# Optimization experiments

Measured on AMD Instinct MI355X. Metric: run time of the kernel, lower is better.

The kernel has to match this reference:

```python
import jax, jax.numpy as jnp
import numpy as np

EPS = 1e-5
HIDDEN = 32

def layer_norm(x, gamma, beta):
    mu = jnp.mean(x, axis=-1, keepdims=True)
    var = jnp.mean(jnp.square(x - mu), axis=-1, keepdims=True)
    return (x - mu) * jax.lax.rsqrt(var + EPS) * gamma + beta

def setup_inputs() -> dict:
    key = jax.random.key(0)
    ks = jax.random.split(key, 5)
    dim, hidden, out_dim = 256, HIDDEN, 128
    B, L = 1, 384
    x = jax.random.normal(ks[0], (B, L, dim), dtype=jnp.float32)
    gamma = jnp.ones((dim,), dtype=jnp.float32)
    beta = jnp.zeros((dim,), dtype=jnp.float32)
    Wa = jax.random.normal(ks[1], (hidden, dim), dtype=jnp.float32) / np.sqrt(dim)
    Wb = jax.random.normal(ks[2], (hidden, dim), dtype=jnp.float32) / np.sqrt(dim)
    Wo = jax.random.normal(ks[3], (out_dim, hidden * hidden), dtype=jnp.float32) / np.sqrt(hidden * hidden)
    bo = jnp.zeros((out_dim,), dtype=jnp.float32)
    return {"x": x, "gamma": gamma, "beta": beta, "Wa": Wa, "Wb": Wb, "Wo": Wo, "bo": bo}

def reference(x, gamma, beta, Wa, Wb, Wo, bo):
    # x: (B, L, dim)
    xn = layer_norm(x, gamma, beta)
    a = jnp.einsum('bld,hd->blh', xn, Wa)  # (B, L, hidden)
    b = jnp.einsum('bld,hd->blh', xn, Wb)  # (B, L, hidden)
    # Reassociated contraction: z[b,i,j,o] = sum_{c,d} a[b,i,c] b[b,j,d] Wo[o, c*H+d]
    # Mathematically identical to materializing the (B,L,L,H*H) outer product.
    Wr = Wo.reshape(Wo.shape[0], HIDDEN, HIDDEN)  # (out, c, d)
    z = jnp.einsum('bic,bjd,ocd->bijo', a, b, Wr) + bo  # (B, L, L, out)
    return z
```

## Files before the change

### kernel.cpp

```cpp
#include <hip/hip_runtime.h>

#define LSEQ 384
#define DIM 256
#define H 32
#define ODIM 128
#define EPSV 1e-5f

__global__ __launch_bounds__(256) void ln_ab_t_kernel(
    const float* __restrict__ x, const float* __restrict__ gamma,
    const float* __restrict__ beta, const float* __restrict__ Wa,
    const float* __restrict__ Wb, const float* __restrict__ Wo,
    float* __restrict__ bT_g, float* __restrict__ t_g) {
  const int i0 = blockIdx.x * 2;
  const int tid = threadIdx.x;
  __shared__ float xn_s[2][DIM];
  __shared__ float psum[2][256];
  __shared__ float red_s[2][4];
  __shared__ float mu_s[2], rs_s[2];
  __shared__ float a_s[2][H];

  const float xv0 = x[i0 * DIM + tid];
  const float xv1 = x[(i0 + 1) * DIM + tid];
  const int wave = tid >> 6, lane = tid & 63;

  float s0 = xv0, s1 = xv1;
#pragma unroll
  for (int off = 32; off > 0; off >>= 1) {
    s0 += __shfl_down(s0, off, 64);
    s1 += __shfl_down(s1, off, 64);
  }
  if (lane == 0) { red_s[0][wave] = s0; red_s[1][wave] = s1; }
  __syncthreads();
  if (tid < 2)
    mu_s[tid] = (red_s[tid][0] + red_s[tid][1] + red_s[tid][2] + red_s[tid][3]) * (1.0f / DIM);
  __syncthreads();
  const float dv0 = xv0 - mu_s[0];
  const float dv1 = xv1 - mu_s[1];

  float q0 = dv0 * dv0, q1 = dv1 * dv1;
#pragma unroll
  for (int off = 32; off > 0; off >>= 1) {
    q0 += __shfl_down(q0, off, 64);
    q1 += __shfl_down(q1, off, 64);
  }
  if (lane == 0) { red_s[0][wave] = q0; red_s[1][wave] = q1; }
  __syncthreads();
  if (tid < 2)
    rs_s[tid] = rsqrtf((red_s[tid][0] + red_s[tid][1] + red_s[tid][2] + red_s[tid][3]) * (1.0f / DIM) + EPSV);
  __syncthreads();

  const float g = gamma[tid], bb = beta[tid];
  xn_s[0][tid] = dv0 * rs_s[0] * g + bb;
  xn_s[1][tid] = dv1 * rs_s[1] * g + bb;
  __syncthreads();

  {
    const int out = tid >> 2;
    const int part = tid & 3;
    const int which = out >> 5;
    const int c = out & 31;
    const float* W = which ? Wb : Wa;
    const float4* Wrow = (const float4*)(W + c * DIM);
    const float4* xn40 = (const float4*)&xn_s[0][0];
    const float4* xn41 = (const float4*)&xn_s[1][0];
    float acc0 = 0.f, acc1 = 0.f;
#pragma unroll
    for (int k = part * 16; k < part * 16 + 16; ++k) {
      const float4 w = Wrow[k];
      const float4 x0 = xn40[k];
      const float4 x1 = xn41[k];
      acc0 += w.x * x0.x + w.y * x0.y + w.z * x0.z + w.w * x0.w;
      acc1 += w.x * x1.x + w.y * x1.y + w.z * x1.z + w.w * x1.w;
    }
    psum[0][tid] = acc0;
    psum[1][tid] = acc1;
  }
  __syncthreads();
  if (tid < 128) {
    const int row = tid >> 6;
    const int out = tid & 63;
    const float v = psum[row][out * 4] + psum[row][out * 4 + 1] +
                    psum[row][out * 4 + 2] + psum[row][out * 4 + 3];
    const int wh = out >> 5, cc = out & 31;
    if (wh == 0) a_s[row][cc] = v;
    else         bT_g[cc * LSEQ + i0 + row] = v;
  }
  __syncthreads();

  const int o = tid >> 1;
  const int dh = tid & 1;
  float4 acc[2][4];
#pragma unroll
  for (int ii = 0; ii < 2; ++ii)
#pragma unroll
    for (int gg = 0; gg < 4; ++gg) acc[ii][gg] = make_float4(0.f, 0.f, 0.f, 0.f);

  const float4* W4 = (const float4*)Wo;
#pragma unroll 4
  for (int c = 0; c < H; ++c) {
    const int base = o * 256 + c * 8 + dh * 4;
    const float a0 = a_s[0][c];
    const float a1 = a_s[1][c];
#pragma unroll
    for (int gg = 0; gg < 4; ++gg) {
      const float4 w = W4[base + gg];
      acc[0][gg].x += a0 * w.x; acc[0][gg].y += a0 * w.y;
      acc[0][gg].z += a0 * w.z; acc[0][gg].w += a0 * w.w;
      acc[1][gg].x += a1 * w.x; acc[1][gg].y += a1 * w.y;
      acc[1][gg].z += a1 * w.z; acc[1][gg].w += a1 * w.w;
    }
  }

  float4* t4 = (float4*)t_g;
#pragma unroll
  for (int ii = 0; ii < 2; ++ii) {
    const int b4 = (i0 + ii) * (ODIM * H / 4) + o * 8 + dh * 4;
#pragma unroll
    for (int gg = 0; gg < 4; ++gg) t4[b4 + gg] = acc[ii][gg];
  }
}

#define FMA4(A, S, T)                                        \
  do {                                                       \
    (A).x += (S) * (T).x; (A).y += (S) * (T).y;              \
    (A).z += (S) * (T).z; (A).w += (S) * (T).w;              \
  } while (0)

__global__ __launch_bounds__(256) void z_kernel(
    const float* __restrict__ t_g, const float* __restrict__ bT_g,
    const float* __restrict__ bo, float* __restrict__ z) {
  const int i = blockIdx.x;
  const int jt = blockIdx.y;
  const int tid = threadIdx.x;
  const int ot = tid & 15;
  const int jg = tid >> 4;

  __shared__ float tt[H][132];
  __shared__ float bt[H][128];

  const float4* t4 = (const float4*)(t_g + i * (ODIM * H));
#pragma unroll
  for (int k = 0; k < 4; ++k) {
    const int f = tid + k * 256;
    const float4 v = t4[f];
    const int o = f >> 3;
    const int d = (f & 7) * 4;
    tt[d][o] = v.x; tt[d + 1][o] = v.y; tt[d + 2][o] = v.z; tt[d + 3][o] = v.w;
  }
#pragma unroll
  for (int k = 0; k < 4; ++k) {
    const int idx4 = tid + k * 256;
    const int d = idx4 >> 5, c4 = idx4 & 31;
    const float4 v = *(const float4*)(bT_g + d * LSEQ + jt * 128 + c4 * 4);
    *(float4*)&bt[d][c4 * 4] = v;
  }
  __syncthreads();

  const float4 bo0 = ((const float4*)bo)[ot];
  const float4 bo1 = ((const float4*)bo)[16 + ot];
  float4 acc0[8], acc1[8];
#pragma unroll
  for (int jj = 0; jj < 8; ++jj) { acc0[jj] = bo0; acc1[jj] = bo1; }

#pragma unroll
  for (int d = 0; d < H; ++d) {
    const float4 tv0 = *(const float4*)&tt[d][ot * 4];
    const float4 tv1 = *(const float4*)&tt[d][64 + ot * 4];
    const float4 b0 = *(const float4*)&bt[d][jg * 8];
    const float4 b1 = *(const float4*)&bt[d][jg * 8 + 4];
    FMA4(acc0[0], b0.x, tv0); FMA4(acc1[0], b0.x, tv1);
    FMA4(acc0[1], b0.y, tv0); FMA4(acc1[1], b0.y, tv1);
    FMA4(acc0[2], b0.z, tv0); FMA4(acc1[2], b0.z, tv1);
    FMA4(acc0[3], b0.w, tv0); FMA4(acc1[3], b0.w, tv1);
    FMA4(acc0[4], b1.x, tv0); FMA4(acc1[4], b1.x, tv1);
    FMA4(acc0[5], b1.y, tv0); FMA4(acc1[5], b1.y, tv1);
    FMA4(acc0[6], b1.z, tv0); FMA4(acc1[6], b1.z, tv1);
    FMA4(acc0[7], b1.w, tv0); FMA4(acc1[7], b1.w, tv1);
  }

  float4* z4 = (float4*)z;
  const int jbase = jt * 128 + jg * 8;
#pragma unroll
  for (int jj = 0; jj < 8; ++jj) {
    const size_t row = (size_t)(i * LSEQ + jbase + jj) * 32;
    z4[row + ot] = acc0[jj];
    z4[row + 16 + ot] = acc1[jj];
  }
}

extern "C" void kernel_launch(void* const* d_in, const int* in_sizes, int n_in,
                              void* d_out, int out_size, void* d_ws, size_t ws_size,
                              hipStream_t stream) {
  const float* x     = (const float*)d_in[0];
  const float* gamma = (const float*)d_in[1];
  const float* beta  = (const float*)d_in[2];
  const float* Wa    = (const float*)d_in[3];
  const float* Wb    = (const float*)d_in[4];
  const float* Wo    = (const float*)d_in[5];
  const float* bo    = (const float*)d_in[6];
  float* z = (float*)d_out;

  float* ws   = (float*)d_ws;
  float* bT_g = ws;
  float* t_g  = ws + LSEQ * H;

  hipLaunchKernelGGL(ln_ab_t_kernel, dim3(LSEQ / 2), dim3(256), 0, stream,
                     x, gamma, beta, Wa, Wb, Wo, bT_g, t_g);
  hipLaunchKernelGGL(z_kernel, dim3(LSEQ, LSEQ / 128), dim3(256), 0, stream,
                     t_g, bT_g, bo, z);
}
```

Baseline: 129.3 us.

## Split first kernel over output halves and enlarge z-kernel j tile

The LN/projection kernel now launches two blocks per row pair, each computing half of the output channels of the t intermediate. This doubles parallelism but recomputes the layer norm and projections in both blocks. The z kernel's j tile grows from 128 to 192, so each thread holds 12 j accumulators instead of 8, with a launch-bounds occupancy hint. This reuses each loaded t tile across more j values and halves the number of z blocks, in exchange for higher register pressure.

Measured after the change: 150.3 us. 16.2% more time.

```diff
diff --git a/kernel.cpp b/kernel.cpp
--- a/kernel.cpp
+++ b/kernel.cpp
@@ -5,13 +5,22 @@
 #define H 32
 #define ODIM 128
 #define EPSV 1e-5f
+#define JT 192
+
+#define FMA4(A, S, T)                                        \
+  do {                                                       \
+    (A).x += (S) * (T).x; (A).y += (S) * (T).y;              \
+    (A).z += (S) * (T).z; (A).w += (S) * (T).w;              \
+  } while (0)
 
 __global__ __launch_bounds__(256) void ln_ab_t_kernel(
     const float* __restrict__ x, const float* __restrict__ gamma,
     const float* __restrict__ beta, const float* __restrict__ Wa,
     const float* __restrict__ Wb, const float* __restrict__ Wo,
     float* __restrict__ bT_g, float* __restrict__ t_g) {
-  const int i0 = blockIdx.x * 2;
+  const int ipair = blockIdx.x >> 1;
+  const int ohalf = blockIdx.x & 1;
+  const int i0 = ipair * 2;
   const int tid = threadIdx.x;
   __shared__ float xn_s[2][DIM];
   __shared__ float psum[2][256];
@@ -83,50 +92,39 @@
                     psum[row][out * 4 + 2] + psum[row][out * 4 + 3];
     const int wh = out >> 5, cc = out & 31;
     if (wh == 0) a_s[row][cc] = v;
-    else         bT_g[cc * LSEQ + i0 + row] = v;
-  }
-  __syncthreads();
-
-  const int o = tid >> 1;
-  const int dh = tid & 1;
-  float4 acc[2][4];
-#pragma unroll
-  for (int ii = 0; ii < 2; ++ii)
-#pragma unroll
-    for (int gg = 0; gg < 4; ++gg) acc[ii][gg] = make_float4(0.f, 0.f, 0.f, 0.f);
+    else if (ohalf == 0) bT_g[cc * LSEQ + i0 + row] = v;
+  }
+  __syncthreads();
+
+  const int ol = tid >> 2;
+  const int dq = tid & 3;
+  const int o = ohalf * 64 + ol;
+
+  float4 acc00 = make_float4(0.f, 0.f, 0.f, 0.f);
+  float4 acc01 = make_float4(0.f, 0.f, 0.f, 0.f);
+  float4 acc10 = make_float4(0.f, 0.f, 0.f, 0.f);
+  float4 acc11 = make_float4(0.f, 0.f, 0.f, 0.f);
 
   const float4* W4 = (const float4*)Wo;
-#pragma unroll 4
+#pragma unroll 8
   for (int c = 0; c < H; ++c) {
-    const int base = o * 256 + c * 8 + dh * 4;
+    const int base = o * 256 + c * 8 + dq * 2;
+    const float4 w0 = W4[base];
+    const float4 w1 = W4[base + 1];
     const float a0 = a_s[0][c];
     const float a1 = a_s[1][c];
-#pragma unroll
-    for (int gg = 0; gg < 4; ++gg) {
-      const float4 w = W4[base + gg];
-      acc[0][gg].x += a0 * w.x; acc[0][gg].y += a0 * w.y;
-      acc[0][gg].z += a0 * w.z; acc[0][gg].w += a0 * w.w;
-      acc[1][gg].x += a1 * w.x; acc[1][gg].y += a1 * w.y;
-      acc[1][gg].z += a1 * w.z; acc[1][gg].w += a1 * w.w;
-    }
+    FMA4(acc00, a0, w0); FMA4(acc01, a0, w1);
+    FMA4(acc10, a1, w0); FMA4(acc11, a1, w1);
   }
 
   float4* t4 = (float4*)t_g;
-#pragma unroll
-  for (int ii = 0; ii < 2; ++ii) {
-    const int b4 = (i0 + ii) * (ODIM * H / 4) + o * 8 + dh * 4;
-#pragma unroll
-    for (int gg = 0; gg < 4; ++gg) t4[b4 + gg] = acc[ii][gg];
-  }
+  const int b40 = i0 * (ODIM * H / 4) + o * 8 + dq * 2;
+  const int b41 = (i0 + 1) * (ODIM * H / 4) + o * 8 + dq * 2;
+  t4[b40] = acc00; t4[b40 + 1] = acc01;
+  t4[b41] = acc10; t4[b41 + 1] = acc11;
 }
 
-#define FMA4(A, S, T)                                        \
-  do {                                                       \
-    (A).x += (S) * (T).x; (A).y += (S) * (T).y;              \
-    (A).z += (S) * (T).z; (A).w += (S) * (T).w;              \
-  } while (0)
-
-__global__ __launch_bounds__(256) void z_kernel(
+__global__ __launch_bounds__(256, 3) void z_kernel(
     const float* __restrict__ t_g, const float* __restrict__ bT_g,
     const float* __restrict__ bo, float* __restrict__ z) {
   const int i = blockIdx.x;
@@ -136,7 +134,7 @@
   const int jg = tid >> 4;
 
   __shared__ float tt[H][132];
-  __shared__ float bt[H][128];
+  __shared__ float bt[H][JT];
 
   const float4* t4 = (const float4*)(t_g + i * (ODIM * H));
 #pragma unroll
@@ -147,41 +145,50 @@
     const int d = (f & 7) * 4;
     tt[d][o] = v.x; tt[d + 1][o] = v.y; tt[d + 2][o] = v.z; tt[d + 3][o] = v.w;
   }
-#pragma unroll
-  for (int k = 0; k < 4; ++k) {
-    const int idx4 = tid + k * 256;
-    const int d = idx4 >> 5, c4 = idx4 & 31;
-    const float4 v = *(const float4*)(bT_g + d * LSEQ + jt * 128 + c4 * 4);
-    *(float4*)&bt[d][c4 * 4] = v;
+  {
+    const int d = tid >> 3;
+    const int c0 = tid & 7;
+    const float* src = bT_g + d * LSEQ + jt * JT;
+#pragma unroll
+    for (int k = 0; k < 6; ++k) {
+      const int c4 = c0 + k * 8;
+      const float4 v = *(const float4*)(src + c4 * 4);
+      *(float4*)&bt[d][c4 * 4] = v;
+    }
   }
   __syncthreads();
 
   const float4 bo0 = ((const float4*)bo)[ot];
   const float4 bo1 = ((const float4*)bo)[16 + ot];
-  float4 acc0[8], acc1[8];
-#pragma unroll
-  for (int jj = 0; jj < 8; ++jj) { acc0[jj] = bo0; acc1[jj] = bo1; }
-
-#pragma unroll
+  float4 acc0[12], acc1[12];
+#pragma unroll
+  for (int jj = 0; jj < 12; ++jj) { acc0[jj] = bo0; acc1[jj] = bo1; }
+
+#pragma unroll 8
   for (int d = 0; d < H; ++d) {
     const float4 tv0 = *(const float4*)&tt[d][ot * 4];
     const float4 tv1 = *(const float4*)&tt[d][64 + ot * 4];
-    const float4 b0 = *(const float4*)&bt[d][jg * 8];
-    const float4 b1 = *(const float4*)&bt[d][jg * 8 + 4];
-    FMA4(acc0[0], b0.x, tv0); FMA4(acc1[0], b0.x, tv1);
-    FMA4(acc0[1], b0.y, tv0); FMA4(acc1[1], b0.y, tv1);
-    FMA4(acc0[2], b0.z, tv0); FMA4(acc1[2], b0.z, tv1);
-    FMA4(acc0[3], b0.w, tv0); FMA4(acc1[3], b0.w, tv1);
-    FMA4(acc0[4], b1.x, tv0); FMA4(acc1[4], b1.x, tv1);
-    FMA4(acc0[5], b1.y, tv0); FMA4(acc1[5], b1.y, tv1);
-    FMA4(acc0[6], b1.z, tv0); FMA4(acc1[6], b1.z, tv1);
-    FMA4(acc0[7], b1.w, tv0); FMA4(acc1[7], b1.w, tv1);
+    const float4 b0 = *(const float4*)&bt[d][jg * 12];
+    const float4 b1 = *(const float4*)&bt[d][jg * 12 + 4];
+    const float4 b2 = *(const float4*)&bt[d][jg * 12 + 8];
+    FMA4(acc0[0], b0.x, tv0);  FMA4(acc1[0], b0.x, tv1);
+    FMA4(acc0[1], b0.y, tv0);  FMA4(acc1[1], b0.y, tv1);
+    FMA4(acc0[2], b0.z, tv0);  FMA4(acc1[2], b0.z, tv1);
+    FMA4(acc0[3], b0.w, tv0);  FMA4(acc1[3], b0.w, tv1);
+    FMA4(acc0[4], b1.x, tv0);  FMA4(acc1[4], b1.x, tv1);
+    FMA4(acc0[5], b1.y, tv0);  FMA4(acc1[5], b1.y, tv1);
+    FMA4(acc0[6], b1.z, tv0);  FMA4(acc1[6], b1.z, tv1);
+    FMA4(acc0[7], b1.w, tv0);  FMA4(acc1[7], b1.w, tv1);
+    FMA4(acc0[8], b2.x, tv0);  FMA4(acc1[8], b2.x, tv1);
+    FMA4(acc0[9], b2.y, tv0);  FMA4(acc1[9], b2.y, tv1);
+    FMA4(acc0[10], b2.z, tv0); FMA4(acc1[10], b2.z, tv1);
+    FMA4(acc0[11], b2.w, tv0); FMA4(acc1[11], b2.w, tv1);
   }
 
   float4* z4 = (float4*)z;
-  const int jbase = jt * 128 + jg * 8;
-#pragma unroll
-  for (int jj = 0; jj < 8; ++jj) {
+  const int jbase = jt * JT + jg * 12;
+#pragma unroll
+  for (int jj = 0; jj < 12; ++jj) {
     const size_t row = (size_t)(i * LSEQ + jbase + jj) * 32;
     z4[row + ot] = acc0[jj];
     z4[row + 16 + ot] = acc1[jj];
@@ -204,8 +211,8 @@
   float* bT_g = ws;
   float* t_g  = ws + LSEQ * H;
 
-  hipLaunchKernelGGL(ln_ab_t_kernel, dim3(LSEQ / 2), dim3(256), 0, stream,
+  hipLaunchKernelGGL(ln_ab_t_kernel, dim3(LSEQ), dim3(256), 0, stream,
                      x, gamma, beta, Wa, Wb, Wo, bT_g, t_g);
-  hipLaunchKernelGGL(z_kernel, dim3(LSEQ, LSEQ / 128), dim3(256), 0, stream,
+  hipLaunchKernelGGL(z_kernel, dim3(LSEQ, LSEQ / JT), dim3(256), 0, stream,
                      t_g, bT_g, bo, z);
 }
```

## Split t computation across two blocks per row pair and store t transposed

Applied to the files above, without the earlier changes.

The first kernel now launches two blocks per pair of rows, each computing half of the output channels of t, which doubles the block count for better occupancy at the cost of recomputing layernorm and the a/b projections in each block. The t intermediate is written directly in d-major (transposed) layout, so the z kernel can copy it into shared memory with plain float4 loads instead of a scattered transpose. In exchange the first kernel's global stores become scalar strided writes.

After: 120.9 us. 1.07x faster.

```diff
diff --git a/kernel.cpp b/kernel.cpp
--- a/kernel.cpp
+++ b/kernel.cpp
@@ -6,12 +6,20 @@
 #define ODIM 128
 #define EPSV 1e-5f
 
+#define FMA4(A, S, T)                                        \
+  do {                                                       \
+    (A).x += (S) * (T).x; (A).y += (S) * (T).y;              \
+    (A).z += (S) * (T).z; (A).w += (S) * (T).w;              \
+  } while (0)
+
 __global__ __launch_bounds__(256) void ln_ab_t_kernel(
     const float* __restrict__ x, const float* __restrict__ gamma,
     const float* __restrict__ beta, const float* __restrict__ Wa,
     const float* __restrict__ Wb, const float* __restrict__ Wo,
     float* __restrict__ bT_g, float* __restrict__ t_g) {
-  const int i0 = blockIdx.x * 2;
+  const int ipair = blockIdx.x >> 1;
+  const int ohalf = blockIdx.x & 1;
+  const int i0 = ipair * 2;
   const int tid = threadIdx.x;
   __shared__ float xn_s[2][DIM];
   __shared__ float psum[2][256];
@@ -83,48 +91,43 @@
                     psum[row][out * 4 + 2] + psum[row][out * 4 + 3];
     const int wh = out >> 5, cc = out & 31;
     if (wh == 0) a_s[row][cc] = v;
-    else         bT_g[cc * LSEQ + i0 + row] = v;
-  }
-  __syncthreads();
-
-  const int o = tid >> 1;
-  const int dh = tid & 1;
-  float4 acc[2][4];
-#pragma unroll
-  for (int ii = 0; ii < 2; ++ii)
-#pragma unroll
-    for (int gg = 0; gg < 4; ++gg) acc[ii][gg] = make_float4(0.f, 0.f, 0.f, 0.f);
+    else if (ohalf == 0) bT_g[cc * LSEQ + i0 + row] = v;
+  }
+  __syncthreads();
+
+  const int ol = tid >> 2;
+  const int dq = tid & 3;
+  const int o = ohalf * 64 + ol;
+
+  float4 acc00 = make_float4(0.f, 0.f, 0.f, 0.f);
+  float4 acc01 = make_float4(0.f, 0.f, 0.f, 0.f);
+  float4 acc10 = make_float4(0.f, 0.f, 0.f, 0.f);
+  float4 acc11 = make_float4(0.f, 0.f, 0.f, 0.f);
 
   const float4* W4 = (const float4*)Wo;
-#pragma unroll 4
+#pragma unroll 8
   for (int c = 0; c < H; ++c) {
-    const int base = o * 256 + c * 8 + dh * 4;
+    const int base = o * 256 + c * 8 + dq * 2;
+    const float4 w0 = W4[base];
+    const float4 w1 = W4[base + 1];
     const float a0 = a_s[0][c];
     const float a1 = a_s[1][c];
-#pragma unroll
-    for (int gg = 0; gg < 4; ++gg) {
-      const float4 w = W4[base + gg];
-      acc[0][gg].x += a0 * w.x; acc[0][gg].y += a0 * w.y;
-      acc[0][gg].z += a0 * w.z; acc[0][gg].w += a0 * w.w;
-      acc[1][gg].x += a1 * w.x; acc[1][gg].y += a1 * w.y;
-      acc[1][gg].z += a1 * w.z; acc[1][gg].w += a1 * w.w;
-    }
-  }
-
-  float4* t4 = (float4*)t_g;
-#pragma unroll
-  for (int ii = 0; ii < 2; ++ii) {
-    const int b4 = (i0 + ii) * (ODIM * H / 4) + o * 8 + dh * 4;
-#pragma unroll
-    for (int gg = 0; gg < 4; ++gg) t4[b4 + gg] = acc[ii][gg];
-  }
+    FMA4(acc00, a0, w0); FMA4(acc01, a0, w1);
+    FMA4(acc10, a1, w0); FMA4(acc11, a1, w1);
+  }
+
+  float* tp0 = t_g + i0 * (H * ODIM) + o;
+  float* tp1 = tp0 + H * ODIM;
+  const int d0 = dq * 8;
+  tp0[(d0 + 0) * ODIM] = acc00.x; tp0[(d0 + 1) * ODIM] = acc00.y;
+  tp0[(d0 + 2) * ODIM] = acc00.z; tp0[(d0 + 3) * ODIM] = acc00.w;
+  tp0[(d0 + 4) * ODIM] = acc01.x; tp0[(d0 + 5) * ODIM] = acc01.y;
+  tp0[(d0 + 6) * ODIM] = acc01.z; tp0[(d0 + 7) * ODIM] = acc01.w;
+  tp1[(d0 + 0) * ODIM] = acc10.x; tp1[(d0 + 1) * ODIM] = acc10.y;
+  tp1[(d0 + 2) * ODIM] = acc10.z; tp1[(d0 + 3) * ODIM] = acc10.w;
+  tp1[(d0 + 4) * ODIM] = acc11.x; tp1[(d0 + 5) * ODIM] = acc11.y;
+  tp1[(d0 + 6) * ODIM] = acc11.z; tp1[(d0 + 7) * ODIM] = acc11.w;
 }
-
-#define FMA4(A, S, T)                                        \
-  do {                                                       \
-    (A).x += (S) * (T).x; (A).y += (S) * (T).y;              \
-    (A).z += (S) * (T).z; (A).w += (S) * (T).w;              \
-  } while (0)
 
 __global__ __launch_bounds__(256) void z_kernel(
     const float* __restrict__ t_g, const float* __restrict__ bT_g,
@@ -135,18 +138,14 @@
   const int ot = tid & 15;
   const int jg = tid >> 4;
 
-  __shared__ float tt[H][132];
+  __shared__ float tt[H][128];
   __shared__ float bt[H][128];
 
   const float4* t4 = (const float4*)(t_g + i * (ODIM * H));
-#pragma unroll
-  for (int k = 0; k < 4; ++k) {
-    const int f = tid + k * 256;
-    const float4 v = t4[f];
-    const int o = f >> 3;
-    const int d = (f & 7) * 4;
-    tt[d][o] = v.x; tt[d + 1][o] = v.y; tt[d + 2][o] = v.z; tt[d + 3][o] = v.w;
-  }
+  float4* ttl = (float4*)&tt[0][0];
+#pragma unroll
+  for (int k = 0; k < 4; ++k) ttl[tid + k * 256] = t4[tid + k * 256];
+
 #pragma unroll
   for (int k = 0; k < 4; ++k) {
     const int idx4 = tid + k * 256;
@@ -204,7 +203,7 @@
   float* bT_g = ws;
   float* t_g  = ws + LSEQ * H;
 
-  hipLaunchKernelGGL(ln_ab_t_kernel, dim3(LSEQ / 2), dim3(256), 0, stream,
+  hipLaunchKernelGGL(ln_ab_t_kernel, dim3(LSEQ), dim3(256), 0, stream,
                      x, gamma, beta, Wa, Wb, Wo, bT_g, t_g);
   hipLaunchKernelGGL(z_kernel, dim3(LSEQ, LSEQ / 128), dim3(256), 0, stream,
                      t_g, bT_g, bo, z);
```
